# Kernel optimization log

Hardware: AMD Instinct MI355X
Metric: run time of the kernel (lower is better)

## Reference

```python
import jax, jax.numpy as jnp
import numpy as np

SIGMA = 0.1
GAMMA = 1.0 / (SIGMA * SIGMA)  # keops-style gauss kernel: exp(-|x-y|^2 / sigma^2)
B, N, D = 1, 8192, 3


def setup_inputs() -> dict:
    key = jax.random.key(0)
    k1, k2 = jax.random.split(key)
    control_points = jax.random.uniform(k1, (B, N, D), dtype=jnp.float32)
    mom = jax.random.normal(k2, (B, N, D), dtype=jnp.float32) * 0.1
    return {"mom": mom, "control_points": control_points}


def _pairwise_dist2(x, y):
    # x:[B,N,D], y:[B,M,D] -> [B,N,M] squared distances (no N x M x D intermediate)
    x2 = jnp.sum(x * x, -1)  # [B,N]
    y2 = jnp.sum(y * y, -1)  # [B,M]
    xy = jnp.einsum('bnd,bmd->bnm', x, y)
    return x2[:, :, None] + y2[:, None, :] - 2.0 * xy


def gauss_kernel(x, y, b):
    # K(x,y) b : [B,N,d]
    K = jnp.exp(-GAMMA * _pairwise_dist2(x, y))  # [B,N,M]
    return jnp.einsum('bnm,bmd->bnd', K, b)


def gauss_grad_kernel(p, x):
    # dH/dx_i = sum_j d/dx_i[exp(-g|x_i-x_j|^2)] <p_i,p_j>
    #         = -2g * sum_j K_ij <p_i,p_j> (x_i - x_j)
    K = jnp.exp(-GAMMA * _pairwise_dist2(x, x))        # [B,N,N]
    W = K * jnp.einsum('bnd,bmd->bnm', p, p)           # [B,N,N] weighted by <p_i,p_j>
    row_sum = jnp.sum(W, -1)                           # [B,N]
    Wx = jnp.einsum('bnm,bmd->bnd', W, x)              # [B,N,D]
    return (-2.0 * GAMMA) * (x * row_sum[:, :, None] - Wx)


def reference(mom, control_points):
    # variational_evolve: (dp/dt, dx/dt)
    dmom = -gauss_grad_kernel(mom, control_points)
    dx = gauss_kernel(control_points, control_points, mom)
    return (dmom, dx)
```

## Files before the change

### kernel.cpp

```cpp
#include <hip/hip_runtime.h>


#define TPB 256
#define ITILE 2
constexpr float GAMMA_C = 100.0f;
constexpr float LOG2E_C = 1.4426950408889634f;
constexpr float SB_C    = 2.0f * GAMMA_C * LOG2E_C;
constexpr float SC_C    = -GAMMA_C * LOG2E_C;
constexpr float LN2_C   = 0.69314718055994531f;

__global__ __launch_bounds__(TPB, 4) void lddmm_partial(
    const float* __restrict__ mom, const float* __restrict__ xpt,
    float* __restrict__ ws, int N, int SEG, int JT) {
  extern __shared__ float4 smem[];
  float4* sA = smem;
  float4* sP = smem + JT;
  const int tid = threadIdx.x;
  const int seg = blockIdx.y;

  for (int t = tid; t < JT; t += TPB) {
    const int j = seg * JT + t;
    const float bx = xpt[3*j], by = xpt[3*j+1], bz = xpt[3*j+2];
    sA[t] = make_float4(SB_C*bx, SB_C*by, SB_C*bz,
                        SC_C * fmaf(bx, bx, fmaf(by, by, bz*bz)));
    sP[t] = make_float4(mom[3*j], mom[3*j+1], mom[3*j+2], 0.f);
  }
  __syncthreads();

  const int i0 = blockIdx.x * (TPB * ITILE) + tid;
  const int i1 = i0 + TPB;

  const float x0 = xpt[3*i0], y0 = xpt[3*i0+1], z0 = xpt[3*i0+2];
  const float p0x = mom[3*i0], p0y = mom[3*i0+1], p0z = mom[3*i0+2];
  const float c0 = SC_C * fmaf(x0, x0, fmaf(y0, y0, z0*z0));
  const float x1 = xpt[3*i1], y1 = xpt[3*i1+1], z1 = xpt[3*i1+2];
  const float p1x = mom[3*i1], p1y = mom[3*i1+1], p1z = mom[3*i1+2];
  const float c1 = SC_C * fmaf(x1, x1, fmaf(y1, y1, z1*z1));

  float a0=0.f, wx0=0.f, wy0=0.f, wz0=0.f, gx0=0.f, gy0=0.f, gz0=0.f;
  float a1=0.f, wx1=0.f, wy1=0.f, wz1=0.f, gx1=0.f, gy1=0.f, gz1=0.f;

#pragma unroll 4
  for (int t = 0; t < JT; ++t) {
    const float4 A = sA[t];
    const float4 P = sP[t];
    {
      const float arg = fmaf(A.x, x0, fmaf(A.y, y0, fmaf(A.z, z0, c0 + A.w)));
      const float K   = __builtin_amdgcn_exp2f(arg);
      const float dot = fmaf(P.x, p0x, fmaf(P.y, p0y, P.z * p0z));
      const float w   = K * dot;
      a0 += w;
      wx0 = fmaf(w, A.x, wx0); wy0 = fmaf(w, A.y, wy0); wz0 = fmaf(w, A.z, wz0);
      gx0 = fmaf(K, P.x, gx0); gy0 = fmaf(K, P.y, gy0); gz0 = fmaf(K, P.z, gz0);
    }
    {
      const float arg = fmaf(A.x, x1, fmaf(A.y, y1, fmaf(A.z, z1, c1 + A.w)));
      const float K   = __builtin_amdgcn_exp2f(arg);
      const float dot = fmaf(P.x, p1x, fmaf(P.y, p1y, P.z * p1z));
      const float w   = K * dot;
      a1 += w;
      wx1 = fmaf(w, A.x, wx1); wy1 = fmaf(w, A.y, wy1); wz1 = fmaf(w, A.z, wz1);
      gx1 = fmaf(K, P.x, gx1); gy1 = fmaf(K, P.y, gy1); gz1 = fmaf(K, P.z, gz1);
    }
  }

  const size_t SN = (size_t)SEG * N;
  float* p = ws + (size_t)seg * N;
  p[0*SN+i0] = a0;  p[0*SN+i1] = a1;
  p[1*SN+i0] = wx0; p[1*SN+i1] = wx1;
  p[2*SN+i0] = wy0; p[2*SN+i1] = wy1;
  p[3*SN+i0] = wz0; p[3*SN+i1] = wz1;
  p[4*SN+i0] = gx0; p[4*SN+i1] = gx1;
  p[5*SN+i0] = gy0; p[5*SN+i1] = gy1;
  p[6*SN+i0] = gz0; p[6*SN+i1] = gz1;
}

__global__ __launch_bounds__(TPB) void lddmm_reduce(
    const float* __restrict__ ws, float* __restrict__ R, int N, int SEG) {
  const int i = blockIdx.x * TPB + threadIdx.x;
  const int c = blockIdx.y;
  const float* src = ws + (size_t)c * SEG * N + i;
  float s0 = 0.f, s1 = 0.f, s2 = 0.f, s3 = 0.f;
  int s = 0;
  for (; s + 4 <= SEG; s += 4) {
    s0 += src[(size_t)(s+0)*N]; s1 += src[(size_t)(s+1)*N];
    s2 += src[(size_t)(s+2)*N]; s3 += src[(size_t)(s+3)*N];
  }
  for (; s < SEG; ++s) s0 += src[(size_t)s*N];
  R[(size_t)c * N + i] = (s0 + s1) + (s2 + s3);
}

__global__ __launch_bounds__(TPB) void lddmm_finalize(
    const float* __restrict__ R, const float* __restrict__ xpt,
    float* __restrict__ out, int N) {
  const int i = blockIdx.x * TPB + threadIdx.x;
  const float A  = R[i];
  const float WX = R[(size_t)1*N+i], WY = R[(size_t)2*N+i], WZ = R[(size_t)3*N+i];
  const float GX = R[(size_t)4*N+i], GY = R[(size_t)5*N+i], GZ = R[(size_t)6*N+i];
  const float xi = xpt[3*i], yi = xpt[3*i+1], zi = xpt[3*i+2];
  const float TGA = 2.0f * GAMMA_C * A;
  out[3*i+0] = fmaf(TGA, xi, -LN2_C * WX);
  out[3*i+1] = fmaf(TGA, yi, -LN2_C * WY);
  out[3*i+2] = fmaf(TGA, zi, -LN2_C * WZ);
  out[3*N + 3*i + 0] = GX;
  out[3*N + 3*i + 1] = GY;
  out[3*N + 3*i + 2] = GZ;
}

__global__ __launch_bounds__(TPB) void lddmm_atomic(
    const float* __restrict__ mom, const float* __restrict__ xpt,
    float* __restrict__ out, int N) {
  const int i  = blockIdx.x * TPB + threadIdx.x;
  const int jb = blockIdx.y * TPB;
  __shared__ float4 sA[TPB], sP[TPB];
  {
    const int j = jb + threadIdx.x;
    const float bx = xpt[3*j], by = xpt[3*j+1], bz = xpt[3*j+2];
    sA[threadIdx.x] = make_float4(SB_C*bx, SB_C*by, SB_C*bz,
                                  SC_C * fmaf(bx, bx, fmaf(by, by, bz*bz)));
    sP[threadIdx.x] = make_float4(mom[3*j], mom[3*j+1], mom[3*j+2], 0.f);
  }
  __syncthreads();
  const float xi = xpt[3*i], yi = xpt[3*i+1], zi = xpt[3*i+2];
  const float pxi = mom[3*i], pyi = mom[3*i+1], pzi = mom[3*i+2];
  const float ci = SC_C * fmaf(xi, xi, fmaf(yi, yi, zi*zi));
  float a=0.f, wx=0.f, wy=0.f, wz=0.f, gx=0.f, gy=0.f, gz=0.f;
#pragma unroll 4
  for (int t = 0; t < TPB; ++t) {
    const float4 A = sA[t], P = sP[t];
    const float arg = fmaf(A.x, xi, fmaf(A.y, yi, fmaf(A.z, zi, ci + A.w)));
    const float K   = __builtin_amdgcn_exp2f(arg);
    const float dot = fmaf(P.x, pxi, fmaf(P.y, pyi, P.z * pzi));
    const float w   = K * dot;
    a += w;
    wx = fmaf(w, A.x, wx); wy = fmaf(w, A.y, wy); wz = fmaf(w, A.z, wz);
    gx = fmaf(K, P.x, gx); gy = fmaf(K, P.y, gy); gz = fmaf(K, P.z, gz);
  }
  const float TGA = 2.0f * GAMMA_C * a;
  atomicAdd(&out[3*i+0], fmaf(TGA, xi, -LN2_C * wx));
  atomicAdd(&out[3*i+1], fmaf(TGA, yi, -LN2_C * wy));
  atomicAdd(&out[3*i+2], fmaf(TGA, zi, -LN2_C * wz));
  atomicAdd(&out[3*N+3*i+0], gx);
  atomicAdd(&out[3*N+3*i+1], gy);
  atomicAdd(&out[3*N+3*i+2], gz);
}

extern "C" void kernel_launch(void* const* d_in, const int* in_sizes, int n_in,
                              void* d_out, int out_size, void* d_ws, size_t ws_size,
                              hipStream_t stream) {
  const float* mom = (const float*)d_in[0];
  const float* xpt = (const float*)d_in[1];
  float* out = (float*)d_out;
  const int N = in_sizes[0] / 3;

  auto need = [&](int s) { return (size_t)(7*s + 7) * (size_t)N * sizeof(float); };
  int SEG = 64;
  while (SEG > 2 && need(SEG) > ws_size) SEG >>= 1;

  if (need(SEG) <= ws_size) {
    const int JT = N / SEG;
    float* wsf = (float*)d_ws;
    float* R   = wsf + (size_t)7 * SEG * N;
    const size_t shmem = (size_t)JT * 2 * sizeof(float4);
    dim3 gA(N / (TPB * ITILE), SEG);
    lddmm_partial<<<gA, TPB, shmem, stream>>>(mom, xpt, wsf, N, SEG, JT);
    dim3 gB(N / TPB, 7);
    lddmm_reduce<<<gB, TPB, 0, stream>>>(wsf, R, N, SEG);
    lddmm_finalize<<<N / TPB, TPB, 0, stream>>>(R, xpt, out, N);
  } else {
    hipMemsetAsync(d_out, 0, (size_t)out_size * sizeof(float), stream);
    dim3 grid(N / TPB, N / TPB);
    lddmm_atomic<<<grid, TPB, 0, stream>>>(mom, xpt, out, N);
  }
}
```

Measured before the change: 96.89 us.

## Precompute j-point table globally, drop LDS staging, fuse reduce and finalize

A new prep kernel writes the scaled coordinates and momenta for every point into a global float4 table once. The partial kernel then reads the table directly through wave-uniform (scalar/broadcast) global loads instead of staging it in shared memory behind a barrier. The reduce and finalize kernels are merged into one, which removes a launch and the intermediate R buffer. SEG is raised to 128 and occupancy hints to 6, giving more blocks but more partial data to reduce. The risk is that global or scalar-cache loads in the inner loop are slower than LDS reads.

```diff
diff --git a/kernel.cpp b/kernel.cpp
--- a/kernel.cpp
+++ b/kernel.cpp
@@ -9,23 +9,23 @@
 constexpr float SC_C    = -GAMMA_C * LOG2E_C;
 constexpr float LN2_C   = 0.69314718055994531f;
 
-__global__ __launch_bounds__(TPB, 4) void lddmm_partial(
+__global__ __launch_bounds__(TPB) void lddmm_prep(
     const float* __restrict__ mom, const float* __restrict__ xpt,
-    float* __restrict__ ws, int N, int SEG, int JT) {
-  extern __shared__ float4 smem[];
-  float4* sA = smem;
-  float4* sP = smem + JT;
+    float4* __restrict__ J, int N) {
+  const int i = blockIdx.x * TPB + threadIdx.x;
+  if (i >= N) return;
+  const float bx = xpt[3*i], by = xpt[3*i+1], bz = xpt[3*i+2];
+  J[2*i]   = make_float4(SB_C*bx, SB_C*by, SB_C*bz,
+                         SC_C * fmaf(bx, bx, fmaf(by, by, bz*bz)));
+  J[2*i+1] = make_float4(mom[3*i], mom[3*i+1], mom[3*i+2], 0.f);
+}
+
+__global__ __launch_bounds__(TPB, 6) void lddmm_partial(
+    const float* __restrict__ mom, const float* __restrict__ xpt,
+    const float4* __restrict__ J,
+    float* __restrict__ part, int N, int SEG, int JT) {
   const int tid = threadIdx.x;
   const int seg = blockIdx.y;
-
-  for (int t = tid; t < JT; t += TPB) {
-    const int j = seg * JT + t;
-    const float bx = xpt[3*j], by = xpt[3*j+1], bz = xpt[3*j+2];
-    sA[t] = make_float4(SB_C*bx, SB_C*by, SB_C*bz,
-                        SC_C * fmaf(bx, bx, fmaf(by, by, bz*bz)));
-    sP[t] = make_float4(mom[3*j], mom[3*j+1], mom[3*j+2], 0.f);
-  }
-  __syncthreads();
 
   const int i0 = blockIdx.x * (TPB * ITILE) + tid;
   const int i1 = i0 + TPB;
@@ -37,13 +37,15 @@
   const float p1x = mom[3*i1], p1y = mom[3*i1+1], p1z = mom[3*i1+2];
   const float c1 = SC_C * fmaf(x1, x1, fmaf(y1, y1, z1*z1));
 
+  const float4* __restrict__ Jseg = J + (size_t)2 * (size_t)seg * (size_t)JT;
+
   float a0=0.f, wx0=0.f, wy0=0.f, wz0=0.f, gx0=0.f, gy0=0.f, gz0=0.f;
   float a1=0.f, wx1=0.f, wy1=0.f, wz1=0.f, gx1=0.f, gy1=0.f, gz1=0.f;
 
 #pragma unroll 4
   for (int t = 0; t < JT; ++t) {
-    const float4 A = sA[t];
-    const float4 P = sP[t];
+    const float4 A = Jseg[2*t];
+    const float4 P = Jseg[2*t+1];
     {
       const float arg = fmaf(A.x, x0, fmaf(A.y, y0, fmaf(A.z, z0, c0 + A.w)));
       const float K   = __builtin_amdgcn_exp2f(arg);
@@ -65,7 +67,7 @@
   }
 
   const size_t SN = (size_t)SEG * N;
-  float* p = ws + (size_t)seg * N;
+  float* p = part + (size_t)seg * N;
   p[0*SN+i0] = a0;  p[0*SN+i1] = a1;
   p[1*SN+i0] = wx0; p[1*SN+i1] = wx1;
   p[2*SN+i0] = wy0; p[2*SN+i1] = wy1;
@@ -75,28 +77,23 @@
   p[6*SN+i0] = gz0; p[6*SN+i1] = gz1;
 }
 
-__global__ __launch_bounds__(TPB) void lddmm_reduce(
-    const float* __restrict__ ws, float* __restrict__ R, int N, int SEG) {
+__global__ __launch_bounds__(TPB) void lddmm_reduce_fin(
+    const float* __restrict__ part, const float* __restrict__ xpt,
+    float* __restrict__ out, int N, int SEG) {
   const int i = blockIdx.x * TPB + threadIdx.x;
-  const int c = blockIdx.y;
-  const float* src = ws + (size_t)c * SEG * N + i;
-  float s0 = 0.f, s1 = 0.f, s2 = 0.f, s3 = 0.f;
-  int s = 0;
-  for (; s + 4 <= SEG; s += 4) {
-    s0 += src[(size_t)(s+0)*N]; s1 += src[(size_t)(s+1)*N];
-    s2 += src[(size_t)(s+2)*N]; s3 += src[(size_t)(s+3)*N];
+  const size_t SN = (size_t)SEG * N;
+  float acc[7];
+#pragma unroll
+  for (int c = 0; c < 7; ++c) acc[c] = 0.f;
+#pragma unroll 2
+  for (int s = 0; s < SEG; ++s) {
+    const float* p = part + (size_t)s * N + i;
+#pragma unroll
+    for (int c = 0; c < 7; ++c) acc[c] += p[(size_t)c * SN];
   }
-  for (; s < SEG; ++s) s0 += src[(size_t)s*N];
-  R[(size_t)c * N + i] = (s0 + s1) + (s2 + s3);
-}
-
-__global__ __launch_bounds__(TPB) void lddmm_finalize(
-    const float* __restrict__ R, const float* __restrict__ xpt,
-    float* __restrict__ out, int N) {
-  const int i = blockIdx.x * TPB + threadIdx.x;
-  const float A  = R[i];
-  const float WX = R[(size_t)1*N+i], WY = R[(size_t)2*N+i], WZ = R[(size_t)3*N+i];
-  const float GX = R[(size_t)4*N+i], GY = R[(size_t)5*N+i], GZ = R[(size_t)6*N+i];
+  const float A  = acc[0];
+  const float WX = acc[1], WY = acc[2], WZ = acc[3];
+  const float GX = acc[4], GY = acc[5], GZ = acc[6];
   const float xi = xpt[3*i], yi = xpt[3*i+1], zi = xpt[3*i+2];
   const float TGA = 2.0f * GAMMA_C * A;
   out[3*i+0] = fmaf(TGA, xi, -LN2_C * WX);
@@ -153,20 +150,19 @@
   float* out = (float*)d_out;
   const int N = in_sizes[0] / 3;
 
-  auto need = [&](int s) { return (size_t)(7*s + 7) * (size_t)N * sizeof(float); };
-  int SEG = 64;
+  auto need = [&](int s) { return (size_t)(8 + 7*s) * (size_t)N * sizeof(float); };
+  int SEG = 128;
   while (SEG > 2 && need(SEG) > ws_size) SEG >>= 1;
 
-  if (need(SEG) <= ws_size) {
+  const bool shapes_ok = (N % (TPB * ITILE) == 0) && (N % SEG == 0);
+  if (need(SEG) <= ws_size && shapes_ok) {
     const int JT = N / SEG;
-    float* wsf = (float*)d_ws;
-    float* R   = wsf + (size_t)7 * SEG * N;
-    const size_t shmem = (size_t)JT * 2 * sizeof(float4);
+    float4* Jv  = (float4*)d_ws;
+    float* partb = (float*)d_ws + (size_t)8 * N;
+    lddmm_prep<<<(N + TPB - 1) / TPB, TPB, 0, stream>>>(mom, xpt, Jv, N);
     dim3 gA(N / (TPB * ITILE), SEG);
-    lddmm_partial<<<gA, TPB, shmem, stream>>>(mom, xpt, wsf, N, SEG, JT);
-    dim3 gB(N / TPB, 7);
-    lddmm_reduce<<<gB, TPB, 0, stream>>>(wsf, R, N, SEG);
-    lddmm_finalize<<<N / TPB, TPB, 0, stream>>>(R, xpt, out, N);
+    lddmm_partial<<<gA, TPB, 0, stream>>>(mom, xpt, Jv, partb, N, SEG, JT);
+    lddmm_reduce_fin<<<N / TPB, TPB, 0, stream>>>(partb, xpt, out, N, SEG);
   } else {
     hipMemsetAsync(d_out, 0, (size_t)out_size * sizeof(float), stream);
     dim3 grid(N / TPB, N / TPB);
```

After: 115.0 us. +18.7%, slower.

## Derive row sum from momentum-weighted kernel sum and retune partial kernel grid

Applied to the files above, without the earlier changes.

Drops the per-pair accumulation of the weighted row sum and instead recovers it in finalize as p_i · (sum_j K_ij p_j), since <p_i,p_j> factors out of the sum. This removes one add per pair and one of the seven partial arrays, which shrinks the workspace traffic in the reduce. The partial kernel also moves to 512-thread blocks with a launch bound of 8, and SEG starts at 128 instead of 64, which changes the grid shape and reduce depth. A shape check now guards the fast path.

```diff
diff --git a/kernel.cpp b/kernel.cpp
--- a/kernel.cpp
+++ b/kernel.cpp
@@ -2,6 +2,7 @@
 
 
 #define TPB 256
+#define TPBP 512
 #define ITILE 2
 constexpr float GAMMA_C = 100.0f;
 constexpr float LOG2E_C = 1.4426950408889634f;
@@ -9,16 +10,16 @@
 constexpr float SC_C    = -GAMMA_C * LOG2E_C;
 constexpr float LN2_C   = 0.69314718055994531f;
 
-__global__ __launch_bounds__(TPB, 4) void lddmm_partial(
+__global__ __launch_bounds__(TPBP, 8) void lddmm_partial(
     const float* __restrict__ mom, const float* __restrict__ xpt,
-    float* __restrict__ ws, int N, int SEG, int JT) {
+    float* __restrict__ part, int N, int SEG, int JT) {
   extern __shared__ float4 smem[];
   float4* sA = smem;
   float4* sP = smem + JT;
   const int tid = threadIdx.x;
   const int seg = blockIdx.y;
 
-  for (int t = tid; t < JT; t += TPB) {
+  for (int t = tid; t < JT; t += TPBP) {
     const int j = seg * JT + t;
     const float bx = xpt[3*j], by = xpt[3*j+1], bz = xpt[3*j+2];
     sA[t] = make_float4(SB_C*bx, SB_C*by, SB_C*bz,
@@ -27,8 +28,8 @@
   }
   __syncthreads();
 
-  const int i0 = blockIdx.x * (TPB * ITILE) + tid;
-  const int i1 = i0 + TPB;
+  const int i0 = blockIdx.x * (TPBP * ITILE) + tid;
+  const int i1 = i0 + TPBP;
 
   const float x0 = xpt[3*i0], y0 = xpt[3*i0+1], z0 = xpt[3*i0+2];
   const float p0x = mom[3*i0], p0y = mom[3*i0+1], p0z = mom[3*i0+2];
@@ -37,8 +38,8 @@
   const float p1x = mom[3*i1], p1y = mom[3*i1+1], p1z = mom[3*i1+2];
   const float c1 = SC_C * fmaf(x1, x1, fmaf(y1, y1, z1*z1));
 
-  float a0=0.f, wx0=0.f, wy0=0.f, wz0=0.f, gx0=0.f, gy0=0.f, gz0=0.f;
-  float a1=0.f, wx1=0.f, wy1=0.f, wz1=0.f, gx1=0.f, gy1=0.f, gz1=0.f;
+  float wx0=0.f, wy0=0.f, wz0=0.f, gx0=0.f, gy0=0.f, gz0=0.f;
+  float wx1=0.f, wy1=0.f, wz1=0.f, gx1=0.f, gy1=0.f, gz1=0.f;
 
 #pragma unroll 4
   for (int t = 0; t < JT; ++t) {
@@ -49,7 +50,6 @@
       const float K   = __builtin_amdgcn_exp2f(arg);
       const float dot = fmaf(P.x, p0x, fmaf(P.y, p0y, P.z * p0z));
       const float w   = K * dot;
-      a0 += w;
       wx0 = fmaf(w, A.x, wx0); wy0 = fmaf(w, A.y, wy0); wz0 = fmaf(w, A.z, wz0);
       gx0 = fmaf(K, P.x, gx0); gy0 = fmaf(K, P.y, gy0); gz0 = fmaf(K, P.z, gz0);
     }
@@ -58,28 +58,26 @@
       const float K   = __builtin_amdgcn_exp2f(arg);
       const float dot = fmaf(P.x, p1x, fmaf(P.y, p1y, P.z * p1z));
       const float w   = K * dot;
-      a1 += w;
       wx1 = fmaf(w, A.x, wx1); wy1 = fmaf(w, A.y, wy1); wz1 = fmaf(w, A.z, wz1);
       gx1 = fmaf(K, P.x, gx1); gy1 = fmaf(K, P.y, gy1); gz1 = fmaf(K, P.z, gz1);
     }
   }
 
   const size_t SN = (size_t)SEG * N;
-  float* p = ws + (size_t)seg * N;
-  p[0*SN+i0] = a0;  p[0*SN+i1] = a1;
-  p[1*SN+i0] = wx0; p[1*SN+i1] = wx1;
-  p[2*SN+i0] = wy0; p[2*SN+i1] = wy1;
-  p[3*SN+i0] = wz0; p[3*SN+i1] = wz1;
-  p[4*SN+i0] = gx0; p[4*SN+i1] = gx1;
-  p[5*SN+i0] = gy0; p[5*SN+i1] = gy1;
-  p[6*SN+i0] = gz0; p[6*SN+i1] = gz1;
+  float* p = part + (size_t)seg * N;
+  p[0*SN+i0] = wx0; p[0*SN+i1] = wx1;
+  p[1*SN+i0] = wy0; p[1*SN+i1] = wy1;
+  p[2*SN+i0] = wz0; p[2*SN+i1] = wz1;
+  p[3*SN+i0] = gx0; p[3*SN+i1] = gx1;
+  p[4*SN+i0] = gy0; p[4*SN+i1] = gy1;
+  p[5*SN+i0] = gz0; p[5*SN+i1] = gz1;
 }
 
 __global__ __launch_bounds__(TPB) void lddmm_reduce(
-    const float* __restrict__ ws, float* __restrict__ R, int N, int SEG) {
+    const float* __restrict__ part, float* __restrict__ R, int N, int SEG) {
   const int i = blockIdx.x * TPB + threadIdx.x;
   const int c = blockIdx.y;
-  const float* src = ws + (size_t)c * SEG * N + i;
+  const float* src = part + (size_t)c * SEG * N + i;
   float s0 = 0.f, s1 = 0.f, s2 = 0.f, s3 = 0.f;
   int s = 0;
   for (; s + 4 <= SEG; s += 4) {
@@ -92,12 +90,13 @@
 
 __global__ __launch_bounds__(TPB) void lddmm_finalize(
     const float* __restrict__ R, const float* __restrict__ xpt,
-    float* __restrict__ out, int N) {
+    const float* __restrict__ mom, float* __restrict__ out, int N) {
   const int i = blockIdx.x * TPB + threadIdx.x;
-  const float A  = R[i];
-  const float WX = R[(size_t)1*N+i], WY = R[(size_t)2*N+i], WZ = R[(size_t)3*N+i];
-  const float GX = R[(size_t)4*N+i], GY = R[(size_t)5*N+i], GZ = R[(size_t)6*N+i];
+  const float WX = R[(size_t)0*N+i], WY = R[(size_t)1*N+i], WZ = R[(size_t)2*N+i];
+  const float GX = R[(size_t)3*N+i], GY = R[(size_t)4*N+i], GZ = R[(size_t)5*N+i];
   const float xi = xpt[3*i], yi = xpt[3*i+1], zi = xpt[3*i+2];
+  const float px = mom[3*i], py = mom[3*i+1], pz = mom[3*i+2];
+  const float A  = fmaf(px, GX, fmaf(py, GY, pz * GZ));
   const float TGA = 2.0f * GAMMA_C * A;
   out[3*i+0] = fmaf(TGA, xi, -LN2_C * WX);
   out[3*i+1] = fmaf(TGA, yi, -LN2_C * WY);
@@ -153,20 +152,22 @@
   float* out = (float*)d_out;
   const int N = in_sizes[0] / 3;
 
-  auto need = [&](int s) { return (size_t)(7*s + 7) * (size_t)N * sizeof(float); };
-  int SEG = 64;
+  auto need = [&](int s) { return (size_t)(6*s + 6) * (size_t)N * sizeof(float); };
+  int SEG = 128;
   while (SEG > 2 && need(SEG) > ws_size) SEG >>= 1;
 
-  if (need(SEG) <= ws_size) {
+  const bool shapes_ok = (N % (TPBP * ITILE) == 0) && (N % SEG == 0) &&
+                         (N % TPB == 0);
+  if (need(SEG) <= ws_size && shapes_ok) {
     const int JT = N / SEG;
-    float* wsf = (float*)d_ws;
-    float* R   = wsf + (size_t)7 * SEG * N;
+    float* partb = (float*)d_ws;
+    float* R     = partb + (size_t)6 * SEG * N;
     const size_t shmem = (size_t)JT * 2 * sizeof(float4);
-    dim3 gA(N / (TPB * ITILE), SEG);
-    lddmm_partial<<<gA, TPB, shmem, stream>>>(mom, xpt, wsf, N, SEG, JT);
-    dim3 gB(N / TPB, 7);
-    lddmm_reduce<<<gB, TPB, 0, stream>>>(wsf, R, N, SEG);
-    lddmm_finalize<<<N / TPB, TPB, 0, stream>>>(R, xpt, out, N);
+    dim3 gA(N / (TPBP * ITILE), SEG);
+    lddmm_partial<<<gA, TPBP, shmem, stream>>>(mom, xpt, partb, N, SEG, JT);
+    dim3 gB(N / TPB, 6);
+    lddmm_reduce<<<gB, TPB, 0, stream>>>(partb, R, N, SEG);
+    lddmm_finalize<<<N / TPB, TPB, 0, stream>>>(R, xpt, mom, out, N);
   } else {
     hipMemsetAsync(d_out, 0, (size_t)out_size * sizeof(float), stream);
     dim3 grid(N / TPB, N / TPB);
```

Result: slower. 220.7 us (+127.8%).
